# Performance work log

Hardware: AMD Instinct MI355X
Metric: run time of the kernel (lower is better)

The kernel has to match this reference:

```python
import math
import jax, jax.numpy as jnp
import numpy as np

B, S, D, H = 2, 4096, 1024, 16
HD = D // H            # 64 head dim
FFN = 4096             # encoder_ffn_dim = 4*d_model
WIN = 512              # attention_window
w = WIN // 2           # one-sided window = 256
NEG = -1e9


def setup_inputs() -> dict:
    key = jax.random.key(0)
    ks = jax.random.split(key, 16)
    p = lambda k, shape: (jax.random.normal(k, shape, jnp.float32) * 0.02)
    inp = {
        "hidden_states": jax.random.normal(ks[0], (B, S, D), jnp.float32),
        "attention_mask": jnp.zeros((B, S), jnp.float32),
        "layer_head_mask": jnp.ones((H,), jnp.float32),
        "is_index_masked": jnp.zeros((B, S), bool),
        "is_index_global_attn": jnp.zeros((B, S), bool),
        "is_global_attn": 0,
        "Wq": p(ks[1], (D, D)), "bq": jnp.zeros((D,), jnp.float32),
        "Wk": p(ks[2], (D, D)), "bk": jnp.zeros((D,), jnp.float32),
        "Wv": p(ks[3], (D, D)), "bv": jnp.zeros((D,), jnp.float32),
        "Wo": p(ks[4], (D, D)), "bo": jnp.zeros((D,), jnp.float32),
        "ln1_g": jnp.ones((D,), jnp.float32), "ln1_b": jnp.zeros((D,), jnp.float32),
        "W1": p(ks[5], (D, FFN)), "b1": jnp.zeros((FFN,), jnp.float32),
        "W2": p(ks[6], (FFN, D)), "b2": jnp.zeros((D,), jnp.float32),
        "ln2_g": jnp.ones((D,), jnp.float32), "ln2_b": jnp.zeros((D,), jnp.float32),
    }
    return inp


def _ln(x, g, b, eps=1e-5):
    m = x.mean(-1, keepdims=True)
    v = ((x - m) ** 2).mean(-1, keepdims=True)
    return (x - m) * jax.lax.rsqrt(v + eps) * g + b


def _blocks3(x, nb, pad_val=0.0):
    # x: [B, H, S, d] -> [B, H, nb, 3w, d]: key blocks b-1, b, b+1 per query block b
    xp = jnp.pad(x, ((0, 0), (0, 0), (w, w), (0, 0)), constant_values=pad_val)
    xb = xp.reshape(x.shape[0], x.shape[1], nb + 2, w, x.shape[-1])
    return jnp.concatenate([xb[:, :, i:i + nb] for i in range(3)], axis=3)


def _sliding_window_attn(q, k, v, key_mask_add, is_masked_q, head_mask):
    # q,k,v: [B, H, S, hd]; banded attention |i-j| <= w
    b, h, s, hd = q.shape
    nb = s // w
    qb = (q * (1.0 / math.sqrt(hd))).reshape(b, h, nb, w, hd)
    kb = _blocks3(k, nb)
    vb = _blocks3(v, nb)
    scores = jnp.einsum("bhnqd,bhnkd->bhnqk", qb, kb)  # [B,H,nb,w,3w]
    # additive key mask (padding keys get NEG)
    kmp = jnp.pad(key_mask_add, ((0, 0), (w, w)), constant_values=NEG)
    kmp = kmp.reshape(b, nb + 2, w)
    km = jnp.concatenate([kmp[:, i:i + nb] for i in range(3)], axis=2)  # [B,nb,3w]
    scores = scores + km[:, None, :, None, :]
    qi = jnp.arange(w)[:, None]
    ki = jnp.arange(3 * w)[None, :]
    band = jnp.abs(ki - w - qi) <= w  # [w, 3w]
    scores = jnp.where(band, scores, NEG)
    probs = jax.nn.softmax(scores, axis=-1)
    probs = probs * head_mask[None, :, None, None, None]
    probs = jnp.where(is_masked_q.reshape(b, 1, nb, w, 1), 0.0, probs)
    out = jnp.einsum("bhnqk,bhnkd->bhnqd", probs, vb)
    return out.reshape(b, h, s, hd)


def reference(hidden_states, attention_mask, layer_head_mask, is_index_masked,
              is_index_global_attn, is_global_attn,
              Wq, bq, Wk, bk, Wv, bv, Wo, bo, ln1_g, ln1_b,
              W1, b1, W2, b2, ln2_g, ln2_b):
    hs = hidden_states
    split = lambda x: (x).reshape(B, S, H, HD).transpose(0, 2, 1, 3)  # [B,H,S,hd]
    q = split(hs @ Wq + bq)
    k = split(hs @ Wk + bk)
    v = split(hs @ Wv + bv)
    attn = _sliding_window_attn(q, k, v, attention_mask, is_index_masked, layer_head_mask)
    attn = attn.transpose(0, 2, 1, 3).reshape(B, S, D)
    attn = attn @ Wo + bo  # self_attn output projection
    x = _ln(hs + attn, ln1_g, ln1_b)
    h = jax.nn.gelu(x @ W1 + b1, approximate=False)
    h = h @ W2 + b2
    x = _ln(x + h, ln2_g, ln2_b)
    return x
```

## Files before the change

kernel.cpp:

```cpp
#include <hip/hip_runtime.h>


typedef unsigned short ushort_t;
typedef unsigned char uchar_t;
typedef __attribute__((ext_vector_type(8))) short bf16x8;
typedef __attribute__((ext_vector_type(4))) float f32x4;

constexpr int CB  = 2;
constexpr int CS  = 4096;
constexpr int CD  = 1024;
constexpr int CH  = 16;
constexpr int CHD = 64;
constexpr int CF  = 4096;
constexpr int CM  = CB * CS;
constexpr float NEGV = -1e9f;

__device__ __forceinline__ ushort_t f2bf(float f) {
  unsigned u = __float_as_uint(f);
  unsigned r = u + 0x7FFFu + ((u >> 16) & 1u);
  return (ushort_t)(r >> 16);
}
__device__ __forceinline__ float gelu_exact(float x) {
  return 0.5f * x * (1.0f + erff(x * 0.70710678118654752f));
}

__device__ __forceinline__ bf16x8 ldsfrag(const char* lds, int row, int slot) {
  return *(const bf16x8*)(lds + row * 128 + (((slot ^ (row & 7)) << 4)));
}

template <int NROWS>
__device__ __forceinline__ void stage_swz(const ushort_t* __restrict__ src, int stride,
                                          char* lds, int tid) {
  const int lane = tid & 63, w = tid >> 6;
#pragma unroll
  for (int it = 0; it < NROWS / 32; ++it) {
    const int o   = it * 4096 + w * 1024;
    const int eo  = o + lane * 16;
    const int row = eo >> 7;
    const int lslot = ((eo >> 4) & 7) ^ (row & 7);
    const ushort_t* g = src + (size_t)row * stride + lslot * 8;
    __builtin_amdgcn_global_load_lds((const __attribute__((address_space(1))) void*)g,
                                     (__attribute__((address_space(3))) void*)(lds + o),
                                     16, 0, 0);
  }
}

__device__ __forceinline__ void stageC(const ushort_t* __restrict__ gtile, int ldK,
                                       char* ldsT, int chunk, int tid) {
  const int eo   = chunk * 8192 + tid * 16;
  const int row  = eo >> 7;
  const int slot = ((eo >> 4) & 7) ^ (row & 7);
  __builtin_amdgcn_global_load_lds(
      (const __attribute__((address_space(1))) void*)(gtile + (size_t)row * ldK + slot * 8),
      (__attribute__((address_space(3))) void*)(ldsT + eo), 16, 0, 0);
}

template <int MH, int NH, int NPH, int NF, int VM, typename F>
__device__ __forceinline__ void phase8(const char* Ax, const char* Bx,
                                       int wr, int wc, int rl, int kl,
                                       f32x4 (&acc)[8][NF], F stage) {
  bf16x8 af[4][2], bfr[NPH][2];
#pragma unroll
  for (int mf = 0; mf < 4; ++mf)
#pragma unroll
    for (int kk = 0; kk < 2; ++kk)
      af[mf][kk] = ldsfrag(Ax, wr * 128 + (MH * 4 + mf) * 16 + rl, kk * 4 + kl);
#pragma unroll
  for (int nf = 0; nf < NPH; ++nf)
#pragma unroll
    for (int kk = 0; kk < 2; ++kk)
      bfr[nf][kk] = ldsfrag(Bx, wc * (NF * 16) + (NH * NPH + nf) * 16 + rl, kk * 4 + kl);
  stage();
  __builtin_amdgcn_s_barrier();
  asm volatile("s_waitcnt lgkmcnt(0)" ::: "memory");
  __builtin_amdgcn_s_setprio(1);
#pragma unroll
  for (int mf = 0; mf < 4; ++mf)
#pragma unroll
    for (int nf = 0; nf < NPH; ++nf)
#pragma unroll
      for (int kk = 0; kk < 2; ++kk)
        acc[MH * 4 + mf][NH * NPH + nf] = __builtin_amdgcn_mfma_f32_16x16x32_bf16(
            af[mf][kk], bfr[nf][kk], acc[MH * 4 + mf][NH * NPH + nf], 0, 0, 0);
  __builtin_amdgcn_s_setprio(0);
  if constexpr (VM == 0) asm volatile("s_waitcnt vmcnt(0)" ::: "memory");
  if constexpr (VM == 2) asm volatile("s_waitcnt vmcnt(2)" ::: "memory");
  if constexpr (VM == 4) asm volatile("s_waitcnt vmcnt(4)" ::: "memory");
  if constexpr (VM == 6) asm volatile("s_waitcnt vmcnt(6)" ::: "memory");
  __builtin_amdgcn_s_barrier();
}

template <int BN>
__device__ __forceinline__ void run_mainloop(const ushort_t* __restrict__ A,
                                             const ushort_t* __restrict__ Bt,
                                             int K, int bm, int bn, char* lds, int tid,
                                             f32x4 (&acc)[8][BN / 64]) {
  constexpr int NF = BN / 64;
  char* Ab0 = lds;
  char* Bb0 = lds + 32768;
  char* Ab1 = lds + 32768 + BN * 128;
  char* Bb1 = Ab1 + 32768;
  const int lane = tid & 63, wid = tid >> 6;
  const int wr = wid >> 2, wc = wid & 3, rl = lane & 15, kl = lane >> 4;
  const ushort_t* Ao = A + (size_t)bm * K;
  const ushort_t* Bo = Bt + (size_t)bn * K;
  const int NT = K >> 6;

  if constexpr (NF == 4) {
#pragma unroll
    for (int c = 0; c < 4; ++c) stageC(Bo, K, Bb0, c, tid);
#pragma unroll
    for (int c = 0; c < 4; ++c) stageC(Ao, K, Ab0, c, tid);
    asm volatile("s_waitcnt vmcnt(0)" ::: "memory");
  } else {
    stageC(Bo, K, Bb0, 0, tid); stageC(Bo, K, Bb0, 1, tid);
#pragma unroll
    for (int c = 0; c < 4; ++c) stageC(Ao, K, Ab0, c, tid);
    if (NT > 1) {
      stageC(Ao + 64, K, Ab1, 0, tid);
      stageC(Ao + 64, K, Ab1, 2, tid);
      asm volatile("s_waitcnt vmcnt(2)" ::: "memory");
    } else {
      asm volatile("s_waitcnt vmcnt(0)" ::: "memory");
    }
  }
  __builtin_amdgcn_s_barrier();

  for (int m = 0; m < NT; ++m) {
    const int p = m & 1;
    char* Ax = p ? Ab1 : Ab0;  char* Bx = p ? Bb1 : Bb0;
    char* Axn = p ? Ab0 : Ab1; char* Bxn = p ? Bb0 : Bb1;
    const bool s1 = (m + 1 < NT), s2 = (m + 2 < NT);
    const ushort_t* An1 = Ao + (m + 1) * 64;
    const ushort_t* Bn1 = Bo + (m + 1) * 64;
    const ushort_t* An2 = Ao + (m + 2) * 64;
    if constexpr (NF == 4) {
      phase8<0, 0, 2, 4, -1>(Ax, Bx, wr, wc, rl, kl, acc, [&] {
        if (s1) { stageC(Bn1, K, Bxn, 0, tid); stageC(Bn1, K, Bxn, 1, tid);
                  stageC(Bn1, K, Bxn, 2, tid); stageC(Bn1, K, Bxn, 3, tid); } });
      if (s1) phase8<0, 1, 2, 4, 6>(Ax, Bx, wr, wc, rl, kl, acc, [&] {
        stageC(An1, K, Axn, 0, tid); stageC(An1, K, Axn, 2, tid); });
      else    phase8<0, 1, 2, 4, 0>(Ax, Bx, wr, wc, rl, kl, acc, [&] {});
      phase8<1, 0, 2, 4, -1>(Ax, Bx, wr, wc, rl, kl, acc, [&] {
        if (s1) { stageC(An1, K, Axn, 1, tid); stageC(An1, K, Axn, 3, tid); } });
      if (s1) phase8<1, 1, 2, 4, 2>(Ax, Bx, wr, wc, rl, kl, acc, [&] {});
      else    phase8<1, 1, 2, 4, 0>(Ax, Bx, wr, wc, rl, kl, acc, [&] {});
    } else {
      if (s1) phase8<0, 0, 2, 2, 6>(Ax, Bx, wr, wc, rl, kl, acc, [&] {
        stageC(Bn1, K, Bxn, 0, tid); stageC(Bn1, K, Bxn, 1, tid);
        stageC(An1, K, Axn, 1, tid); stageC(An1, K, Axn, 3, tid); });
      else    phase8<0, 0, 2, 2, 0>(Ax, Bx, wr, wc, rl, kl, acc, [&] {});
      if (s2)      phase8<1, 0, 2, 2, 4>(Ax, Bx, wr, wc, rl, kl, acc, [&] {
        stageC(An2, K, Ax, 0, tid); stageC(An2, K, Ax, 2, tid); });
      else if (s1) phase8<1, 0, 2, 2, 2>(Ax, Bx, wr, wc, rl, kl, acc, [&] {});
      else         phase8<1, 0, 2, 2, 0>(Ax, Bx, wr, wc, rl, kl, acc, [&] {});
    }
  }
}

__device__ __forceinline__ void swz_block(int BN, int& bm, int& bn) {
  const int gx = gridDim.x;
  const int nwg = gx * gridDim.y;
  const int id0 = blockIdx.x + gx * blockIdx.y;
  const int wgid = (id0 & 7) * (nwg >> 3) + (id0 >> 3);
  bm = (wgid % gx) * 256;
  bn = (wgid / gx) * BN;
}

template <int BN, int EPI>
__global__ __launch_bounds__(512, 1) void gemm8(
    const ushort_t* __restrict__ A, const ushort_t* __restrict__ Bt,
    const float* __restrict__ bias, const float* __restrict__ res,
    float* __restrict__ outF, ushort_t* __restrict__ outB, int N, int K) {
  constexpr int NF = BN / 64;
  __shared__ __align__(16) char lds[2 * (32768 + BN * 128)];
  const int tid = threadIdx.x;
  int bm, bn; swz_block(BN, bm, bn);
  f32x4 acc[8][NF] = {};
  run_mainloop<BN>(A, Bt, K, bm, bn, lds, tid, acc);
  const int lane = tid & 63, wid = tid >> 6;
  const int wr = wid >> 2, wc = wid & 3, rl = lane & 15, kl = lane >> 4;
#pragma unroll
  for (int mf = 0; mf < 8; ++mf) {
    const int r0 = bm + wr * 128 + mf * 16 + kl * 4;
#pragma unroll
    for (int nf = 0; nf < NF; ++nf) {
      const int col = bn + wc * (NF * 16) + nf * 16 + rl;
      const float bb = bias[col];
#pragma unroll
      for (int i = 0; i < 4; ++i) {
        float v = acc[mf][nf][i] + bb;
        if (EPI == 1) {
          v += res[(size_t)(r0 + i) * N + col];
          outF[(size_t)(r0 + i) * N + col] = v;
        } else {
          outB[(size_t)(r0 + i) * N + col] = f2bf(gelu_exact(v));
        }
      }
    }
  }
}

__global__ __launch_bounds__(512, 1) void qkv8(
    const ushort_t* __restrict__ hsb, const ushort_t* __restrict__ WqkvT,
    const float* __restrict__ bq, const float* __restrict__ bk, const float* __restrict__ bv,
    ushort_t* __restrict__ q, ushort_t* __restrict__ k, ushort_t* __restrict__ vt) {
  __shared__ __align__(16) char lds[2 * (32768 + 16384)];
  const int tid = threadIdx.x;
  int bm, bn; swz_block(128, bm, bn);
  const int which = bn >> 10;
  const int bnl = bn & 1023;
  const float* bia = (which == 0) ? bq : (which == 1) ? bk : bv;
  const float mul  = (which == 0) ? 0.125f : 1.0f;
  f32x4 acc[8][2] = {};
  run_mainloop<128>(hsb, WqkvT, CD, bm, bn, lds, tid, acc);
  const int lane = tid & 63, wid = tid >> 6;
  const int wr = wid >> 2, wc = wid & 3, rl = lane & 15, kl = lane >> 4;
#pragma unroll
  for (int mf = 0; mf < 8; ++mf) {
    const int r0 = bm + wr * 128 + mf * 16 + kl * 4;
    const int bidx = r0 >> 12;
    const int s0 = r0 & (CS - 1);
#pragma unroll
    for (int nf = 0; nf < 2; ++nf) {
      const int col = bnl + wc * 32 + nf * 16 + rl;
      const int h = col >> 6, hd = col & 63;
      const float bb = bia[col];
      if (which < 2) {
        ushort_t* dst = (which == 0 ? q : k);
#pragma unroll
        for (int i = 0; i < 4; ++i) {
          const float v = (acc[mf][nf][i] + bb) * mul;
          dst[((((size_t)bidx * CH + h) * CS) + s0 + i) * CHD + hd] = f2bf(v);
        }
      } else {
        ushort4 o;
        o.x = f2bf(acc[mf][nf][0] + bb); o.y = f2bf(acc[mf][nf][1] + bb);
        o.z = f2bf(acc[mf][nf][2] + bb); o.w = f2bf(acc[mf][nf][3] + bb);
        *(ushort4*)&vt[(((size_t)bidx * CH + h) * CHD + hd) * CS + s0] = o;
      }
    }
  }
}

__global__ __launch_bounds__(256) void cast_bf16(const float* __restrict__ x,
                                                 ushort_t* __restrict__ y) {
  const size_t i = ((size_t)blockIdx.x * 256 + threadIdx.x) * 4;
  const float4 v = *(const float4*)(x + i);
  ushort4 o;
  o.x = f2bf(v.x); o.y = f2bf(v.y); o.z = f2bf(v.z); o.w = f2bf(v.w);
  *(ushort4*)(y + i) = o;
}

__global__ __launch_bounds__(256) void transpose_cast(const float* __restrict__ W,
                                                      ushort_t* __restrict__ Wt,
                                                      int K, int N) {
  __shared__ float t[64][65];
  const int k0 = blockIdx.x * 64, n0 = blockIdx.y * 64;
  const int ty = threadIdx.x >> 4, tx = threadIdx.x & 15;
#pragma unroll
  for (int rr = 0; rr < 4; ++rr) {
    const int r = rr * 16 + ty;
    const float4 v = *(const float4*)&W[(size_t)(k0 + r) * N + n0 + tx * 4];
    t[r][tx * 4 + 0] = v.x; t[r][tx * 4 + 1] = v.y;
    t[r][tx * 4 + 2] = v.z; t[r][tx * 4 + 3] = v.w;
  }
  __syncthreads();
#pragma unroll
  for (int rr = 0; rr < 4; ++rr) {
    const int rn = rr * 16 + ty;
    ushort4 o;
    o.x = f2bf(t[tx * 4 + 0][rn]); o.y = f2bf(t[tx * 4 + 1][rn]);
    o.z = f2bf(t[tx * 4 + 2][rn]); o.w = f2bf(t[tx * 4 + 3][rn]);
    *(ushort4*)&Wt[(size_t)(n0 + rn) * K + k0 + tx * 4] = o;
  }
}

__global__ __launch_bounds__(256) void attn_mfma(
    const ushort_t* __restrict__ qg, const ushort_t* __restrict__ kg,
    const ushort_t* __restrict__ vtg,
    const float* __restrict__ amask, const uchar_t* __restrict__ qmask,
    const float* __restrict__ hmask, ushort_t* __restrict__ outb) {
  __shared__ __align__(16) char Qs[8192];
  __shared__ __align__(16) char Ks[8192];
  __shared__ __align__(16) char Vt[8192];
  __shared__ __align__(16) char Ps[8192];
  const int qt0 = blockIdx.x * 64, h = blockIdx.y, b = blockIdx.z;
  const int tid = threadIdx.x, lane = tid & 63, w = tid >> 6;
  const size_t bh = (size_t)b * CH + h;

  stage_swz<64>(qg + (bh * CS + qt0) * CHD, CHD, Qs, tid);

  f32x4 O[4] = {};
  float m_run[4], l_run[4];
#pragma unroll
  for (int i = 0; i < 4; ++i) { m_run[i] = -INFINITY; l_run[i] = 0.f; }

  for (int c = 0; c < 9; ++c) {
    const int k0 = qt0 - 256 + c * 64;
    if (k0 < 0 || k0 >= CS) continue;
    __syncthreads();
    stage_swz<64>(kg + (bh * CS + k0) * CHD, CHD, Ks, tid);
    stage_swz<64>(vtg + bh * CHD * CS + k0, CS, Vt, tid);
    __syncthreads();

    f32x4 s[4] = {};
#pragma unroll
    for (int kk = 0; kk < 2; ++kk) {
      const bf16x8 a = ldsfrag(Qs, w * 16 + (lane & 15), kk * 4 + (lane >> 4));
#pragma unroll
      for (int n = 0; n < 4; ++n) {
        const bf16x8 bb = ldsfrag(Ks, n * 16 + (lane & 15), kk * 4 + (lane >> 4));
        s[n] = __builtin_amdgcn_mfma_f32_16x16x32_bf16(a, bb, s[n], 0, 0, 0);
      }
    }

    float kmv[4]; int keyc[4];
#pragma unroll
    for (int n = 0; n < 4; ++n) {
      keyc[n] = k0 + n * 16 + (lane & 15);
      kmv[n] = amask[(size_t)b * CS + keyc[n]];
    }
    const int qrb = qt0 + w * 16 + ((lane >> 4) << 2);
#pragma unroll
    for (int i = 0; i < 4; ++i) {
      const int qi = qrb + i;
      float mx = -INFINITY;
#pragma unroll
      for (int n = 0; n < 4; ++n) {
        const int d = keyc[n] - qi;
        float x = (d <= 256 && d >= -256) ? (s[n][i] + kmv[n]) : NEGV;
        s[n][i] = x;
        mx = fmaxf(mx, x);
      }
      mx = fmaxf(mx, __shfl_xor(mx, 1));
      mx = fmaxf(mx, __shfl_xor(mx, 2));
      mx = fmaxf(mx, __shfl_xor(mx, 4));
      mx = fmaxf(mx, __shfl_xor(mx, 8));
      const float m_new = fmaxf(m_run[i], mx);
      const float scf = expf(m_run[i] - m_new);
      float rs = 0.f;
#pragma unroll
      for (int n = 0; n < 4; ++n) {
        const float p = expf(s[n][i] - m_new);
        s[n][i] = p;
        rs += p;
      }
      rs += __shfl_xor(rs, 1); rs += __shfl_xor(rs, 2);
      rs += __shfl_xor(rs, 4); rs += __shfl_xor(rs, 8);
      l_run[i] = l_run[i] * scf + rs;
      m_run[i] = m_new;
#pragma unroll
      for (int n = 0; n < 4; ++n) O[n][i] *= scf;
      const int prow = w * 16 + ((lane >> 4) << 2) + i;
#pragma unroll
      for (int n = 0; n < 4; ++n) {
        const int pcol = n * 16 + (lane & 15);
        const int byte = prow * 128 + ((((pcol >> 3) ^ (prow & 7)) << 4)) + ((pcol & 7) << 1);
        *(ushort_t*)(Ps + byte) = f2bf(s[n][i]);
      }
    }
    __syncthreads();

#pragma unroll
    for (int kk = 0; kk < 2; ++kk) {
      const bf16x8 pa = ldsfrag(Ps, w * 16 + (lane & 15), kk * 4 + (lane >> 4));
#pragma unroll
      for (int nd = 0; nd < 4; ++nd) {
        const bf16x8 vv = ldsfrag(Vt, nd * 16 + (lane & 15), kk * 4 + (lane >> 4));
        O[nd] = __builtin_amdgcn_mfma_f32_16x16x32_bf16(pa, vv, O[nd], 0, 0, 0);
      }
    }
  }

  const float hm = hmask[h];
#pragma unroll
  for (int i = 0; i < 4; ++i) {
    const int qi = qt0 + w * 16 + ((lane >> 4) << 2) + i;
    const bool qm = qmask[(size_t)b * CS + qi] != 0;
    const float scl = (qm ? 0.f : hm) / fmaxf(l_run[i], 1e-30f);
#pragma unroll
    for (int nd = 0; nd < 4; ++nd) {
      const int col = h * CHD + nd * 16 + (lane & 15);
      outb[((size_t)b * CS + qi) * CD + col] = f2bf(O[nd][i] * scl);
    }
  }
}

__global__ __launch_bounds__(256) void ln_f32(const float* __restrict__ X,
                                              const float* __restrict__ g,
                                              const float* __restrict__ bt,
                                              float* __restrict__ Y,
                                              ushort_t* __restrict__ Yb) {
  const int row = blockIdx.x;
  const int tid = threadIdx.x;
  const float4 xv = *(const float4*)(X + (size_t)row * CD + (tid << 2));
  float s  = xv.x + xv.y + xv.z + xv.w;
  float s2 = xv.x * xv.x + xv.y * xv.y + xv.z * xv.z + xv.w * xv.w;
#pragma unroll
  for (int off = 32; off; off >>= 1) {
    s  += __shfl_xor(s, off);
    s2 += __shfl_xor(s2, off);
  }
  __shared__ float red[8];
  const int wv = tid >> 6;
  if ((tid & 63) == 0) { red[wv] = s; red[wv + 4] = s2; }
  __syncthreads();
  s  = red[0] + red[1] + red[2] + red[3];
  s2 = red[4] + red[5] + red[6] + red[7];
  const float mean = s * (1.f / CD);
  const float var  = s2 * (1.f / CD) - mean * mean;
  const float r = rsqrtf(var + 1e-5f);
  const float4 gv = *(const float4*)(g + (tid << 2));
  const float4 bv = *(const float4*)(bt + (tid << 2));
  float4 o;
  o.x = (xv.x - mean) * r * gv.x + bv.x;
  o.y = (xv.y - mean) * r * gv.y + bv.y;
  o.z = (xv.z - mean) * r * gv.z + bv.z;
  o.w = (xv.w - mean) * r * gv.w + bv.w;
  *(float4*)(Y + (size_t)row * CD + (tid << 2)) = o;
  if (Yb) {
    ushort4 ob;
    ob.x = f2bf(o.x); ob.y = f2bf(o.y); ob.z = f2bf(o.z); ob.w = f2bf(o.w);
    *(ushort4*)(Yb + (size_t)row * CD + (tid << 2)) = ob;
  }
}

extern "C" void kernel_launch(void* const* d_in, const int* in_sizes, int n_in,
                              void* d_out, int out_size, void* d_ws, size_t ws_size,
                              hipStream_t stream) {
  const float* hs    = (const float*)d_in[0];
  const float* amask = (const float*)d_in[1];
  const float* hmask = (const float*)d_in[2];
  const uchar_t* qmask = (const uchar_t*)d_in[3];
  const float* Wq = (const float*)d_in[6];
  const float* bq = (const float*)d_in[7];
  const float* Wk = (const float*)d_in[8];
  const float* bk = (const float*)d_in[9];
  const float* Wv = (const float*)d_in[10];
  const float* bv = (const float*)d_in[11];
  const float* Wo = (const float*)d_in[12];
  const float* bo = (const float*)d_in[13];
  const float* ln1g = (const float*)d_in[14];
  const float* ln1b = (const float*)d_in[15];
  const float* W1 = (const float*)d_in[16];
  const float* b1 = (const float*)d_in[17];
  const float* W2 = (const float*)d_in[18];
  const float* b2 = (const float*)d_in[19];
  const float* ln2g = (const float*)d_in[20];
  const float* ln2b = (const float*)d_in[21];

  char* ws = (char*)d_ws;
  const size_t MB = 1024 * 1024;
  ushort_t* hsb   = (ushort_t*)(ws);
  ushort_t* WqkvT = (ushort_t*)(ws + 16 * MB);
  ushort_t* WoT   = (ushort_t*)(ws + 22 * MB);
  ushort_t* W1T   = (ushort_t*)(ws + 24 * MB);
  ushort_t* W2T   = (ushort_t*)(ws + 32 * MB);
  ushort_t* qb    = (ushort_t*)(ws + 40 * MB);
  ushort_t* kb    = (ushort_t*)(ws + 56 * MB);
  ushort_t* vtb   = (ushort_t*)(ws + 72 * MB);
  ushort_t* attb  = (ushort_t*)(ws + 88 * MB);
  float*    tmp   = (float*)(ws + 104 * MB);
  float*    x1    = (float*)(ws + 40 * MB);
  ushort_t* x1b   = (ushort_t*)(ws + 72 * MB);
  ushort_t* hb    = (ushort_t*)(ws + 136 * MB);
  float*    outf  = (float*)d_out;

  cast_bf16<<<(CM * CD) / 1024, 256, 0, stream>>>(hs, hsb);
  transpose_cast<<<dim3(CD / 64, CD / 64), 256, 0, stream>>>(Wq, WqkvT, CD, CD);
  transpose_cast<<<dim3(CD / 64, CD / 64), 256, 0, stream>>>(Wk, WqkvT + 1024 * 1024, CD, CD);
  transpose_cast<<<dim3(CD / 64, CD / 64), 256, 0, stream>>>(Wv, WqkvT + 2 * 1024 * 1024, CD, CD);
  transpose_cast<<<dim3(CD / 64, CD / 64), 256, 0, stream>>>(Wo, WoT, CD, CD);
  transpose_cast<<<dim3(CD / 64, CF / 64), 256, 0, stream>>>(W1, W1T, CD, CF);
  transpose_cast<<<dim3(CF / 64, CD / 64), 256, 0, stream>>>(W2, W2T, CF, CD);

  qkv8<<<dim3(CM / 256, 3072 / 128), 512, 0, stream>>>(
      hsb, WqkvT, bq, bk, bv, qb, kb, vtb);

  attn_mfma<<<dim3(CS / 64, CH, CB), 256, 0, stream>>>(
      qb, kb, vtb, amask, qmask, hmask, attb);

  gemm8<128, 1><<<dim3(CM / 256, CD / 128), 512, 0, stream>>>(
      attb, WoT, bo, hs, tmp, nullptr, CD, CD);

  ln_f32<<<CM, 256, 0, stream>>>(tmp, ln1g, ln1b, x1, x1b);

  gemm8<256, 2><<<dim3(CM / 256, CF / 256), 512, 0, stream>>>(
      x1b, W1T, b1, nullptr, nullptr, hb, CF, CD);

  gemm8<128, 1><<<dim3(CM / 256, CD / 128), 512, 0, stream>>>(
      hb, W2T, b2, x1, outf, nullptr, CD, CF);

  ln_f32<<<CM, 256, 0, stream>>>(outf, ln2g, ln2b, outf, nullptr);
}
```

Measured before the change: 601.8 us.

## Restructure GEMM mainloop into k-split quarter phases and drop block swizzle

Replaces the per-NF specialised phase schedules with a uniform four-phase schedule that splits each 64-wide K tile into two k-halves and two M-halves. B fragments are reused across the two M-halves, which cuts LDS fragment reads. The deeper A-tile prefetch used for narrow tiles is removed. The XCD-aware workgroup swizzle is replaced with plain blockIdx mapping, which may hurt L2 locality.

```diff
diff --git a/kernel.cpp b/kernel.cpp
--- a/kernel.cpp
+++ b/kernel.cpp
@@ -55,38 +55,34 @@
       (__attribute__((address_space(3))) void*)(ldsT + eo), 16, 0, 0);
 }
 
-template <int MH, int NH, int NPH, int NF, int VM, typename F>
-__device__ __forceinline__ void phase8(const char* Ax, const char* Bx,
+template <int NF, int MH, int KK, bool LB, int VM, typename F>
+__device__ __forceinline__ void phaseQ(const char* Ax, const char* Bx,
+                                       bf16x8 (&bfr)[NF],
                                        int wr, int wc, int rl, int kl,
                                        f32x4 (&acc)[8][NF], F stage) {
-  bf16x8 af[4][2], bfr[NPH][2];
-#pragma unroll
-  for (int mf = 0; mf < 4; ++mf)
-#pragma unroll
-    for (int kk = 0; kk < 2; ++kk)
-      af[mf][kk] = ldsfrag(Ax, wr * 128 + (MH * 4 + mf) * 16 + rl, kk * 4 + kl);
-#pragma unroll
-  for (int nf = 0; nf < NPH; ++nf)
-#pragma unroll
-    for (int kk = 0; kk < 2; ++kk)
-      bfr[nf][kk] = ldsfrag(Bx, wc * (NF * 16) + (NH * NPH + nf) * 16 + rl, kk * 4 + kl);
+  bf16x8 a4[4];
+#pragma unroll
+  for (int i = 0; i < 4; ++i)
+    a4[i] = ldsfrag(Ax, wr * 128 + (MH * 4 + i) * 16 + rl, KK * 4 + kl);
+  if constexpr (LB) {
+#pragma unroll
+    for (int nf = 0; nf < NF; ++nf)
+      bfr[nf] = ldsfrag(Bx, wc * (NF * 16) + nf * 16 + rl, KK * 4 + kl);
+  }
   stage();
   __builtin_amdgcn_s_barrier();
   asm volatile("s_waitcnt lgkmcnt(0)" ::: "memory");
   __builtin_amdgcn_s_setprio(1);
 #pragma unroll
-  for (int mf = 0; mf < 4; ++mf)
-#pragma unroll
-    for (int nf = 0; nf < NPH; ++nf)
-#pragma unroll
-      for (int kk = 0; kk < 2; ++kk)
-        acc[MH * 4 + mf][NH * NPH + nf] = __builtin_amdgcn_mfma_f32_16x16x32_bf16(
-            af[mf][kk], bfr[nf][kk], acc[MH * 4 + mf][NH * NPH + nf], 0, 0, 0);
+  for (int i = 0; i < 4; ++i)
+#pragma unroll
+    for (int nf = 0; nf < NF; ++nf)
+      acc[MH * 4 + i][nf] = __builtin_amdgcn_mfma_f32_16x16x32_bf16(
+          a4[i], bfr[nf], acc[MH * 4 + i][nf], 0, 0, 0);
   __builtin_amdgcn_s_setprio(0);
   if constexpr (VM == 0) asm volatile("s_waitcnt vmcnt(0)" ::: "memory");
   if constexpr (VM == 2) asm volatile("s_waitcnt vmcnt(2)" ::: "memory");
   if constexpr (VM == 4) asm volatile("s_waitcnt vmcnt(4)" ::: "memory");
-  if constexpr (VM == 6) asm volatile("s_waitcnt vmcnt(6)" ::: "memory");
   __builtin_amdgcn_s_barrier();
 }
 
@@ -106,65 +102,37 @@
   const ushort_t* Bo = Bt + (size_t)bn * K;
   const int NT = K >> 6;
 
-  if constexpr (NF == 4) {
-#pragma unroll
-    for (int c = 0; c < 4; ++c) stageC(Bo, K, Bb0, c, tid);
-#pragma unroll
-    for (int c = 0; c < 4; ++c) stageC(Ao, K, Ab0, c, tid);
-    asm volatile("s_waitcnt vmcnt(0)" ::: "memory");
-  } else {
-    stageC(Bo, K, Bb0, 0, tid); stageC(Bo, K, Bb0, 1, tid);
-#pragma unroll
-    for (int c = 0; c < 4; ++c) stageC(Ao, K, Ab0, c, tid);
-    if (NT > 1) {
-      stageC(Ao + 64, K, Ab1, 0, tid);
-      stageC(Ao + 64, K, Ab1, 2, tid);
-      asm volatile("s_waitcnt vmcnt(2)" ::: "memory");
-    } else {
-      asm volatile("s_waitcnt vmcnt(0)" ::: "memory");
-    }
-  }
+#pragma unroll
+  for (int c = 0; c < NF; ++c) stageC(Bo, K, Bb0, c, tid);
+  stageC(Ao, K, Ab0, 0, tid); stageC(Ao, K, Ab0, 2, tid);
+  stageC(Ao, K, Ab0, 1, tid); stageC(Ao, K, Ab0, 3, tid);
+  asm volatile("s_waitcnt vmcnt(2)" ::: "memory");
   __builtin_amdgcn_s_barrier();
 
   for (int m = 0; m < NT; ++m) {
     const int p = m & 1;
     char* Ax = p ? Ab1 : Ab0;  char* Bx = p ? Bb1 : Bb0;
     char* Axn = p ? Ab0 : Ab1; char* Bxn = p ? Bb0 : Bb1;
-    const bool s1 = (m + 1 < NT), s2 = (m + 2 < NT);
+    const bool s1 = (m + 1 < NT);
     const ushort_t* An1 = Ao + (m + 1) * 64;
     const ushort_t* Bn1 = Bo + (m + 1) * 64;
-    const ushort_t* An2 = Ao + (m + 2) * 64;
-    if constexpr (NF == 4) {
-      phase8<0, 0, 2, 4, -1>(Ax, Bx, wr, wc, rl, kl, acc, [&] {
-        if (s1) { stageC(Bn1, K, Bxn, 0, tid); stageC(Bn1, K, Bxn, 1, tid);
-                  stageC(Bn1, K, Bxn, 2, tid); stageC(Bn1, K, Bxn, 3, tid); } });
-      if (s1) phase8<0, 1, 2, 4, 6>(Ax, Bx, wr, wc, rl, kl, acc, [&] {
-        stageC(An1, K, Axn, 0, tid); stageC(An1, K, Axn, 2, tid); });
-      else    phase8<0, 1, 2, 4, 0>(Ax, Bx, wr, wc, rl, kl, acc, [&] {});
-      phase8<1, 0, 2, 4, -1>(Ax, Bx, wr, wc, rl, kl, acc, [&] {
-        if (s1) { stageC(An1, K, Axn, 1, tid); stageC(An1, K, Axn, 3, tid); } });
-      if (s1) phase8<1, 1, 2, 4, 2>(Ax, Bx, wr, wc, rl, kl, acc, [&] {});
-      else    phase8<1, 1, 2, 4, 0>(Ax, Bx, wr, wc, rl, kl, acc, [&] {});
+    bf16x8 bfr[NF];
+    if (s1) {
+      phaseQ<NF, 0, 0, true, NF>(Ax, Bx, bfr, wr, wc, rl, kl, acc, [&] {
+#pragma unroll
+        for (int c = 0; c < NF; ++c) stageC(Bn1, K, Bxn, c, tid); });
+      phaseQ<NF, 1, 0, false, -1>(Ax, Bx, bfr, wr, wc, rl, kl, acc, [&] {
+        stageC(An1, K, Axn, 0, tid); stageC(An1, K, Axn, 2, tid);
+        stageC(An1, K, Axn, 1, tid); stageC(An1, K, Axn, 3, tid); });
+      phaseQ<NF, 0, 1, true, -1>(Ax, Bx, bfr, wr, wc, rl, kl, acc, [&] {});
+      phaseQ<NF, 1, 1, false, 2>(Ax, Bx, bfr, wr, wc, rl, kl, acc, [&] {});
     } else {
-      if (s1) phase8<0, 0, 2, 2, 6>(Ax, Bx, wr, wc, rl, kl, acc, [&] {
-        stageC(Bn1, K, Bxn, 0, tid); stageC(Bn1, K, Bxn, 1, tid);
-        stageC(An1, K, Axn, 1, tid); stageC(An1, K, Axn, 3, tid); });
-      else    phase8<0, 0, 2, 2, 0>(Ax, Bx, wr, wc, rl, kl, acc, [&] {});
-      if (s2)      phase8<1, 0, 2, 2, 4>(Ax, Bx, wr, wc, rl, kl, acc, [&] {
-        stageC(An2, K, Ax, 0, tid); stageC(An2, K, Ax, 2, tid); });
-      else if (s1) phase8<1, 0, 2, 2, 2>(Ax, Bx, wr, wc, rl, kl, acc, [&] {});
-      else         phase8<1, 0, 2, 2, 0>(Ax, Bx, wr, wc, rl, kl, acc, [&] {});
-    }
-  }
-}
-
-__device__ __forceinline__ void swz_block(int BN, int& bm, int& bn) {
-  const int gx = gridDim.x;
-  const int nwg = gx * gridDim.y;
-  const int id0 = blockIdx.x + gx * blockIdx.y;
-  const int wgid = (id0 & 7) * (nwg >> 3) + (id0 >> 3);
-  bm = (wgid % gx) * 256;
-  bn = (wgid / gx) * BN;
+      phaseQ<NF, 0, 0, true, 0>(Ax, Bx, bfr, wr, wc, rl, kl, acc, [&] {});
+      phaseQ<NF, 1, 0, false, -1>(Ax, Bx, bfr, wr, wc, rl, kl, acc, [&] {});
+      phaseQ<NF, 0, 1, true, -1>(Ax, Bx, bfr, wr, wc, rl, kl, acc, [&] {});
+      phaseQ<NF, 1, 1, false, -1>(Ax, Bx, bfr, wr, wc, rl, kl, acc, [&] {});
+    }
+  }
 }
 
 template <int BN, int EPI>
@@ -175,7 +143,7 @@
   constexpr int NF = BN / 64;
   __shared__ __align__(16) char lds[2 * (32768 + BN * 128)];
   const int tid = threadIdx.x;
-  int bm, bn; swz_block(BN, bm, bn);
+  const int bm = blockIdx.x * 256, bn = blockIdx.y * BN;
   f32x4 acc[8][NF] = {};
   run_mainloop<BN>(A, Bt, K, bm, bn, lds, tid, acc);
   const int lane = tid & 63, wid = tid >> 6;
@@ -207,7 +175,7 @@
     ushort_t* __restrict__ q, ushort_t* __restrict__ k, ushort_t* __restrict__ vt) {
   __shared__ __align__(16) char lds[2 * (32768 + 16384)];
   const int tid = threadIdx.x;
-  int bm, bn; swz_block(128, bm, bn);
+  const int bm = blockIdx.x * 256, bn = blockIdx.y * 128;
   const int which = bn >> 10;
   const int bnl = bn & 1023;
   const float* bia = (which == 0) ? bq : (which == 1) ? bk : bv;
```

Result: slower. 833.1 us (+38.4%).
